# Kernel tuning notes

Hardware: AMD Instinct MI355X
Metric: run time of the kernel (lower is better)

## Reference

```python
import jax, jax.numpy as jnp
import numpy as np

B = 8192      # batch size
D = 512       # feature dim == num_classes (centers is [C, C] in the original)
C = 512       # num_classes
MARGIN = 1.0


def setup_inputs() -> dict:
    key = jax.random.key(0)
    k1, k2, k3 = jax.random.split(key, 3)
    inputs = jax.random.normal(k1, (B, D), dtype=jnp.float32)
    targets = jax.random.randint(k2, (B,), 0, C)
    centers = jax.random.normal(k3, (C, D), dtype=jnp.float32)  # learned param
    return {"inputs": inputs, "targets": targets, "centers": centers}


def reference(inputs, targets, centers):
    # centers_batch[j] = centers[targets[j]]  (gather rows)
    cb = centers[targets]                                   # [B, D]
    # dist[i, j] = || inputs[i] - cb[j] ||_2, computed via the expanded form
    # (||a||^2 + ||b||^2 - 2 a.b) so we never materialize a [B, B, D] tensor.
    sq = ((inputs * inputs).sum(-1)[:, None]
          + (cb * cb).sum(-1)[None, :]
          - 2.0 * (inputs @ cb.T))                          # [B, B]
    dist = jnp.sqrt(jnp.clip(sq, 1e-12))                    # clamp(min=1e-12).sqrt()

    # mask[i, j] = (targets[i] == targets[j]); note original indexes dist[i][mask[i]]
    mask = targets[:, None] == targets[None, :]             # [B, B] bool
    dist_ap = jnp.max(jnp.where(mask, dist, -jnp.inf), axis=1)   # hardest positive per row
    dist_an = jnp.min(jnp.where(mask, jnp.inf, dist), axis=1)    # hardest negative per row

    # MarginRankingLoss(margin)(dist_an, dist_ap, y=1) = mean(relu(dist_ap - dist_an + margin))
    loss = jnp.mean(jnp.maximum(0.0, dist_ap - dist_an + MARGIN))
    prec = jnp.mean((dist_an > dist_ap).astype(jnp.float32))
    return loss, prec
```

## Files before the change

kernel.cpp:

```cpp
#include <hip/hip_runtime.h>
#include <hip/hip_bf16.h>

#define NB 8192
#define ND 512
#define NC 512
#define NCT 8
#define MARGIN_F 1.0f
#define BIGF 3.0e38f
#define K3_BLOCKS 32

typedef __attribute__((ext_vector_type(8))) short bf16x8;
typedef __attribute__((ext_vector_type(4))) float f32x4;

__device__ __forceinline__ unsigned fkey(float f) {
    unsigned u = __float_as_uint(f);
    unsigned mask = (u & 0x80000000u) ? 0xFFFFFFFFu : 0x80000000u;
    return u ^ mask;
}
__device__ __forceinline__ float finv(unsigned k) {
    unsigned mask = (k & 0x80000000u) ? 0x80000000u : 0xFFFFFFFFu;
    return __uint_as_float(k ^ mask);
}
__device__ __forceinline__ unsigned short f2bf(float f) {
    __hip_bfloat16 h = __float2bfloat16(f);
    return __builtin_bit_cast(unsigned short, h);
}

#define GLOAD_LDS16(g, l)                                                    \
    __builtin_amdgcn_global_load_lds(                                        \
        (const __attribute__((address_space(1))) void*)(g),                  \
        (__attribute__((address_space(3))) void*)(l), 16, 0, 0)

__global__ __launch_bounds__(256) void k0_prep(
    const float* __restrict__ inputs, const int* __restrict__ targets,
    const float* __restrict__ centers,
    unsigned short* __restrict__ inB, unsigned short* __restrict__ cenB,
    float* __restrict__ rsq, float* __restrict__ csq,
    unsigned* __restrict__ counts, unsigned long long* __restrict__ accums)
{
    const int bid = blockIdx.x;
    const int tid = threadIdx.x;

    if (bid == 2176) {
        __shared__ unsigned hist[NC];
        if (tid < 3) accums[tid] = 0ull;
        for (int i = tid; i < NC; i += 256) hist[i] = 0u;
        __syncthreads();
        for (int i = tid; i < NB; i += 256) atomicAdd(&hist[targets[i]], 1u);
        __syncthreads();
        for (int i = tid; i < NC; i += 256) counts[i] = hist[i];
        return;
    }

    const int wave = tid >> 6, lane = tid & 63;
    const float* src;
    unsigned short* dst;
    float* sqdst;
    int row;
    bool is_input = (bid < 2048);
    if (is_input) {
        row   = bid * 4 + wave;
        src   = inputs + (size_t)row * ND;
        dst   = inB + (size_t)row * ND;
        sqdst = rsq + row;
    } else {
        row   = (bid - 2048) * 4 + wave;
        src   = centers + (size_t)row * ND;
        dst   = cenB + (size_t)row * ND;
        sqdst = csq + row;
    }

    float4 v1 = ((const float4*)src)[lane];
    float4 v2 = ((const float4*)src)[lane + 64];
    float s = v1.x*v1.x + v1.y*v1.y + v1.z*v1.z + v1.w*v1.w
            + v2.x*v2.x + v2.y*v2.y + v2.z*v2.z + v2.w*v2.w;

    ushort4 o1, o2;
    o1.x = f2bf(v1.x); o1.y = f2bf(v1.y); o1.z = f2bf(v1.z); o1.w = f2bf(v1.w);
    o2.x = f2bf(v2.x); o2.y = f2bf(v2.y); o2.z = f2bf(v2.z); o2.w = f2bf(v2.w);
    ((ushort4*)dst)[lane]      = o1;
    ((ushort4*)dst)[lane + 64] = o2;

    #pragma unroll
    for (int off = 32; off > 0; off >>= 1) s += __shfl_down(s, off);
    if (lane == 0) *sqdst = s;
}

__global__ __launch_bounds__(256) void k2_mfma(
    const unsigned short* __restrict__ Ain, const unsigned short* __restrict__ cenB,
    const int* __restrict__ targets, const unsigned* __restrict__ counts,
    const float* __restrict__ csq,
    float* __restrict__ partmin, float* __restrict__ apval)
{
    __shared__ __align__(16) unsigned short As[2][128 * 32];
    __shared__ __align__(16) unsigned short Bs[2][64 * 32];
    __shared__ int      tgtL[128];
    __shared__ float    csqL[64];
    __shared__ unsigned ldsmin[128];

    const int tid  = threadIdx.x;
    const int w    = tid >> 6;
    const int lane = tid & 63;
    const int wm   = w >> 1;
    const int wn   = w & 1;
    const int qd   = lane >> 4;
    const int ln   = lane & 15;

    const int bid   = blockIdx.x;
    const int rbase = (bid & 63) * 128;
    const int ct    = bid >> 6;
    const int cbase = ct * 64;

    if (tid < 128) { tgtL[tid] = targets[rbase + tid]; ldsmin[tid] = 0xFFFFFFFFu; }
    if (tid < 64) {
        const int c = cbase + tid;
        csqL[tid] = (counts[c] > 0u) ? csq[c] : BIGF;
    }

    const int arow0 = w * 32 + (lane >> 2);
    const int brow  = w * 16 + (lane >> 2);
    const int scol  = (lane & 3) * 8;
    const unsigned short* gA0 = Ain  + (size_t)(rbase + arow0)      * ND + scol;
    const unsigned short* gA1 = Ain  + (size_t)(rbase + arow0 + 16) * ND + scol;
    const unsigned short* gB  = cenB + (size_t)(cbase + brow)       * ND + scol;

    f32x4 acc[4][2] = {};

#define STAGE(buf, kb) do {                                                  \
        GLOAD_LDS16(gA0 + (kb), &As[buf][(w * 32)      * 32]);               \
        GLOAD_LDS16(gA1 + (kb), &As[buf][(w * 32 + 16) * 32]);               \
        GLOAD_LDS16(gB  + (kb), &Bs[buf][(w * 16)      * 32]);               \
    } while (0)

#define COMPUTE(buf) do {                                                    \
        bf16x8 a[4], b[2];                                                   \
        _Pragma("unroll")                                                    \
        for (int i = 0; i < 4; ++i)                                          \
            a[i] = *(const bf16x8*)&As[buf][(wm * 64 + i * 16 + ln) * 32 + qd * 8]; \
        _Pragma("unroll")                                                    \
        for (int j = 0; j < 2; ++j)                                          \
            b[j] = *(const bf16x8*)&Bs[buf][(wn * 32 + j * 16 + ln) * 32 + qd * 8]; \
        _Pragma("unroll")                                                    \
        for (int i = 0; i < 4; ++i)                                          \
            _Pragma("unroll")                                                \
            for (int j = 0; j < 2; ++j)                                      \
                acc[i][j] = __builtin_amdgcn_mfma_f32_16x16x32_bf16(a[i], b[j], acc[i][j], 0, 0, 0); \
    } while (0)

    STAGE(0, 0);
    __syncthreads();
    int cur = 0;
    #pragma unroll
    for (int kb = 32; kb < ND; kb += 32) {
        STAGE(cur ^ 1, kb);
        COMPUTE(cur);
        __syncthreads();
        cur ^= 1;
    }
    COMPUTE(cur);

    #pragma unroll
    for (int i = 0; i < 4; ++i) {
        #pragma unroll
        for (int r = 0; r < 4; ++r) {
            const int rlocal = wm * 64 + i * 16 + qd * 4 + r;
            const int grow   = rbase + rlocal;
            const int tr     = tgtL[rlocal];
            float m = BIGF;
            #pragma unroll
            for (int j = 0; j < 2; ++j) {
                const int clocal = wn * 32 + j * 16 + ln;
                const float val = csqL[clocal] - 2.0f * acc[i][j][r];
                if (cbase + clocal == tr) {
                    apval[grow] = val;
                } else {
                    m = fminf(m, val);
                }
            }
            #pragma unroll
            for (int off = 1; off < 16; off <<= 1)
                m = fminf(m, __shfl_xor(m, off));
            if (ln == 0) atomicMin(&ldsmin[rlocal], fkey(m));
        }
    }
    __syncthreads();
    if (tid < 128)
        partmin[(size_t)(rbase + tid) * NCT + ct] = finv(ldsmin[tid]);
}

__global__ __launch_bounds__(256) void k3_final(
    const float* __restrict__ rsq, const float* __restrict__ partmin,
    const float* __restrict__ apval, unsigned long long* __restrict__ acc,
    float* __restrict__ out)
{
    const int tid = threadIdx.x;
    const int r   = blockIdx.x * 256 + tid;

    const float4* pm = (const float4*)&partmin[(size_t)r * NCT];
    float4 m0 = pm[0], m1 = pm[1];
    float m = fminf(fminf(fminf(m0.x, m0.y), fminf(m0.z, m0.w)),
                    fminf(fminf(m1.x, m1.y), fminf(m1.z, m1.w)));
    float s  = rsq[r];
    float an = sqrtf(fmaxf(s + m,        1e-12f));
    float ap = sqrtf(fmaxf(s + apval[r], 1e-12f));
    float a = fmaxf(0.0f, ap - an + MARGIN_F);
    float p = (an > ap) ? 1.0f : 0.0f;

    #pragma unroll
    for (int off = 32; off > 0; off >>= 1) {
        a += __shfl_down(a, off);
        p += __shfl_down(p, off);
    }
    __shared__ float sa[4], sp[4];
    const int w = tid >> 6, lane = tid & 63;
    if (lane == 0) { sa[w] = a; sp[w] = p; }
    __syncthreads();
    if (tid == 0) {
        float A = sa[0] + sa[1] + sa[2] + sa[3];
        float P = sp[0] + sp[1] + sp[2] + sp[3];
        atomicAdd(&acc[0], (unsigned long long)((double)A * 4294967296.0 + 0.5));
        atomicAdd(&acc[1], (unsigned long long)(P + 0.5f));
        __threadfence();
        unsigned* ctr = (unsigned*)&acc[2];
        if (atomicAdd(ctr, 1u) == K3_BLOCKS - 1) {
            unsigned long long ls = atomicAdd(&acc[0], 0ull);
            unsigned long long ps = atomicAdd(&acc[1], 0ull);
            out[0] = (float)((double)ls / (4294967296.0 * (double)NB));
            out[1] = (float)((double)ps / (double)NB);
        }
    }
}

extern "C" void kernel_launch(void* const* d_in, const int* in_sizes, int n_in,
                              void* d_out, int out_size, void* d_ws, size_t ws_size,
                              hipStream_t stream) {
    const float* inputs  = (const float*)d_in[0];
    const int*   targets = (const int*)d_in[1];
    const float* centers = (const float*)d_in[2];
    float* out = (float*)d_out;

    char* wp = (char*)d_ws;
    unsigned short* inB     = (unsigned short*)(wp);
    unsigned short* cenB    = (unsigned short*)(wp + 8388608);
    float*          rsq     = (float*)(wp + 8912896);
    float*          csqv    = (float*)(wp + 8945664);
    unsigned*       counts  = (unsigned*)(wp + 8947712);
    float*          apval   = (float*)(wp + 8949760);
    float*          partmin = (float*)(wp + 8982528);
    unsigned long long* accums = (unsigned long long*)(wp + 9244672);

    k0_prep<<<2177, 256, 0, stream>>>(inputs, targets, centers,
                                      inB, cenB, rsq, csqv, counts, accums);
    k2_mfma<<<512, 256, 0, stream>>>(inB, cenB, targets, counts, csqv,
                                     partmin, apval);
    k3_final<<<K3_BLOCKS, 256, 0, stream>>>(rsq, partmin, apval, accums, out);
}
```

Measured before the change: 93.83 us.

## Fuse final reduction into GEMM kernel via atomic min and last-block completion

Removes the separate final-reduction kernel. The GEMM kernel now merges per-row negative minima with global atomicMin into a buffer that the prep kernel initialises. The last of the eight column-tile blocks for each row tile computes loss and precision and adds them into global accumulators, and a global counter picks the block that writes the output. This saves one kernel launch and the partial-min buffer round trip, at the cost of extra global atomics and fences in the GEMM epilogue.

```diff
diff --git a/kernel.cpp b/kernel.cpp
--- a/kernel.cpp
+++ b/kernel.cpp
@@ -4,10 +4,8 @@
 #define NB 8192
 #define ND 512
 #define NC 512
-#define NCT 8
 #define MARGIN_F 1.0f
 #define BIGF 3.0e38f
-#define K3_BLOCKS 32
 
 typedef __attribute__((ext_vector_type(8))) short bf16x8;
 typedef __attribute__((ext_vector_type(4))) float f32x4;
@@ -36,14 +34,16 @@
     const float* __restrict__ centers,
     unsigned short* __restrict__ inB, unsigned short* __restrict__ cenB,
     float* __restrict__ rsq, float* __restrict__ csq,
-    unsigned* __restrict__ counts, unsigned long long* __restrict__ accums)
+    unsigned* __restrict__ counts, unsigned* __restrict__ anG,
+    unsigned* __restrict__ ctrl, unsigned long long* __restrict__ acc2)
 {
     const int bid = blockIdx.x;
     const int tid = threadIdx.x;
 
     if (bid == 2176) {
         __shared__ unsigned hist[NC];
-        if (tid < 3) accums[tid] = 0ull;
+        if (tid < 65) ctrl[tid] = 0u;
+        if (tid == 65) { acc2[0] = 0ull; acc2[1] = 0ull; }
         for (int i = tid; i < NC; i += 256) hist[i] = 0u;
         __syncthreads();
         for (int i = tid; i < NB; i += 256) atomicAdd(&hist[targets[i]], 1u);
@@ -63,6 +63,7 @@
         src   = inputs + (size_t)row * ND;
         dst   = inB + (size_t)row * ND;
         sqdst = rsq + row;
+        if (tid < 4) anG[bid * 4 + tid] = 0xFFFFFFFFu;
     } else {
         row   = (bid - 2048) * 4 + wave;
         src   = centers + (size_t)row * ND;
@@ -89,14 +90,18 @@
 __global__ __launch_bounds__(256) void k2_mfma(
     const unsigned short* __restrict__ Ain, const unsigned short* __restrict__ cenB,
     const int* __restrict__ targets, const unsigned* __restrict__ counts,
-    const float* __restrict__ csq,
-    float* __restrict__ partmin, float* __restrict__ apval)
+    const float* __restrict__ csq, const float* __restrict__ rsq,
+    unsigned* __restrict__ anG, float* __restrict__ apG,
+    unsigned* __restrict__ ctrl, unsigned long long* __restrict__ acc2,
+    float* __restrict__ out)
 {
     __shared__ __align__(16) unsigned short As[2][128 * 32];
     __shared__ __align__(16) unsigned short Bs[2][64 * 32];
     __shared__ int      tgtL[128];
     __shared__ float    csqL[64];
     __shared__ unsigned ldsmin[128];
+    __shared__ double   fa[4], fp_[4];
+    __shared__ int      isfin;
 
     const int tid  = threadIdx.x;
     const int w    = tid >> 6;
@@ -107,7 +112,8 @@
     const int ln   = lane & 15;
 
     const int bid   = blockIdx.x;
-    const int rbase = (bid & 63) * 128;
+    const int rt    = bid & 63;
+    const int rbase = rt * 128;
     const int ct    = bid >> 6;
     const int cbase = ct * 64;
 
@@ -172,7 +178,7 @@
                 const int clocal = wn * 32 + j * 16 + ln;
                 const float val = csqL[clocal] - 2.0f * acc[i][j][r];
                 if (cbase + clocal == tr) {
-                    apval[grow] = val;
+                    apG[grow] = val;
                 } else {
                     m = fminf(m, val);
                 }
@@ -185,46 +191,46 @@
     }
     __syncthreads();
     if (tid < 128)
-        partmin[(size_t)(rbase + tid) * NCT + ct] = finv(ldsmin[tid]);
-}
-
-__global__ __launch_bounds__(256) void k3_final(
-    const float* __restrict__ rsq, const float* __restrict__ partmin,
-    const float* __restrict__ apval, unsigned long long* __restrict__ acc,
-    float* __restrict__ out)
-{
-    const int tid = threadIdx.x;
-    const int r   = blockIdx.x * 256 + tid;
-
-    const float4* pm = (const float4*)&partmin[(size_t)r * NCT];
-    float4 m0 = pm[0], m1 = pm[1];
-    float m = fminf(fminf(fminf(m0.x, m0.y), fminf(m0.z, m0.w)),
-                    fminf(fminf(m1.x, m1.y), fminf(m1.z, m1.w)));
-    float s  = rsq[r];
-    float an = sqrtf(fmaxf(s + m,        1e-12f));
-    float ap = sqrtf(fmaxf(s + apval[r], 1e-12f));
-    float a = fmaxf(0.0f, ap - an + MARGIN_F);
-    float p = (an > ap) ? 1.0f : 0.0f;
-
+        atomicMin(&anG[rbase + tid], ldsmin[tid]);
+
+    if (tid == 0) {
+        __threadfence();
+        isfin = (atomicAdd(&ctrl[rt], 1u) == 7u) ? 1 : 0;
+    }
+    __syncthreads();
+    if (!isfin) return;
+
+    __threadfence();
+    double a = 0.0, p = 0.0;
+    if (tid < 128) {
+        const int r = rbase + tid;
+        const unsigned ank = atomicMin(&anG[r], 0xFFFFFFFFu);
+        const unsigned apu = atomicOr((unsigned*)apG + r, 0u);
+        const float mv  = finv(ank);
+        const float apv = __uint_as_float(apu);
+        const float s   = rsq[r];
+        const float an  = sqrtf(fmaxf(s + mv,  1e-12f));
+        const float ap  = sqrtf(fmaxf(s + apv, 1e-12f));
+        a = (double)fmaxf(0.0f, ap - an + MARGIN_F);
+        p = (an > ap) ? 1.0 : 0.0;
+    }
     #pragma unroll
     for (int off = 32; off > 0; off >>= 1) {
         a += __shfl_down(a, off);
         p += __shfl_down(p, off);
     }
-    __shared__ float sa[4], sp[4];
-    const int w = tid >> 6, lane = tid & 63;
-    if (lane == 0) { sa[w] = a; sp[w] = p; }
+    if (lane == 0) { fa[w] = a; fp_[w] = p; }
     __syncthreads();
     if (tid == 0) {
-        float A = sa[0] + sa[1] + sa[2] + sa[3];
-        float P = sp[0] + sp[1] + sp[2] + sp[3];
-        atomicAdd(&acc[0], (unsigned long long)((double)A * 4294967296.0 + 0.5));
-        atomicAdd(&acc[1], (unsigned long long)(P + 0.5f));
+        const double A = fa[0] + fa[1] + fa[2] + fa[3];
+        const double P = fp_[0] + fp_[1] + fp_[2] + fp_[3];
+        atomicAdd(&acc2[0], (unsigned long long)(A * 4294967296.0 + 0.5));
+        atomicAdd(&acc2[1], (unsigned long long)(P + 0.5));
         __threadfence();
-        unsigned* ctr = (unsigned*)&acc[2];
-        if (atomicAdd(ctr, 1u) == K3_BLOCKS - 1) {
-            unsigned long long ls = atomicAdd(&acc[0], 0ull);
-            unsigned long long ps = atomicAdd(&acc[1], 0ull);
+        unsigned* gctr = &ctrl[64];
+        if (atomicAdd(gctr, 1u) == 63u) {
+            unsigned long long ls = atomicAdd(&acc2[0], 0ull);
+            unsigned long long ps = atomicAdd(&acc2[1], 0ull);
             out[0] = (float)((double)ls / (4294967296.0 * (double)NB));
             out[1] = (float)((double)ps / (double)NB);
         }
@@ -240,18 +246,19 @@
     float* out = (float*)d_out;
 
     char* wp = (char*)d_ws;
-    unsigned short* inB     = (unsigned short*)(wp);
-    unsigned short* cenB    = (unsigned short*)(wp + 8388608);
-    float*          rsq     = (float*)(wp + 8912896);
-    float*          csqv    = (float*)(wp + 8945664);
-    unsigned*       counts  = (unsigned*)(wp + 8947712);
-    float*          apval   = (float*)(wp + 8949760);
-    float*          partmin = (float*)(wp + 8982528);
-    unsigned long long* accums = (unsigned long long*)(wp + 9244672);
+    unsigned short* inB    = (unsigned short*)(wp);
+    unsigned short* cenB   = (unsigned short*)(wp + 8388608);
+    float*          rsq    = (float*)(wp + 8912896);
+    float*          csqv   = (float*)(wp + 8945664);
+    unsigned*       counts = (unsigned*)(wp + 8947712);
+    float*          apG    = (float*)(wp + 8949760);
+    unsigned*       anG    = (unsigned*)(wp + 8982528);
+    unsigned*       ctrl   = (unsigned*)(wp + 9015296);
+    unsigned long long* acc2 = (unsigned long long*)(wp + 9015808);
 
     k0_prep<<<2177, 256, 0, stream>>>(inputs, targets, centers,
-                                      inB, cenB, rsq, csqv, counts, accums);
-    k2_mfma<<<512, 256, 0, stream>>>(inB, cenB, targets, counts, csqv,
-                                     partmin, apval);
-    k3_final<<<K3_BLOCKS, 256, 0, stream>>>(rsq, partmin, apval, accums, out);
-}
+                                      inB, cenB, rsq, csqv, counts,
+                                      anG, ctrl, acc2);
+    k2_mfma<<<512, 256, 0, stream>>>(inB, cenB, targets, counts, csqv, rsq,
+                                     anG, apG, ctrl, acc2, out);
+}
```

New measurement: 103.7 us. +10.5%, slower.
